# Performance work log

Hardware: AMD Instinct MI355X
Metric: run time of the kernel (lower is better)

Reference implementation:

```python
import jax, jax.numpy as jnp
import numpy as np

N_NODES = 100000


def gcn_conv(x, W, b, src, dst, deg_inv_sqrt):
    # x: [N, Cin], W: [Cin, Cout]. PyG GCNConv: transform then normalized aggregate.
    h = x @ W  # [N, Cout]
    norm = deg_inv_sqrt[src] * deg_inv_sqrt[dst]  # [E']
    msg = h[src] * norm[:, None]  # gather + scale
    out = jax.ops.segment_sum(msg, dst, num_segments=N_NODES)
    return out + b


def setup_inputs() -> dict:
    key = jax.random.key(0)
    ks = jax.random.split(key, 8)
    C = 256
    E = 3200000
    x = jax.random.normal(ks[0], (N_NODES, C), dtype=jnp.float32)
    edge_index = jax.random.randint(ks[1], (2, E), 0, N_NODES, dtype=jnp.int64)
    s = 1.0 / np.sqrt(C)
    W1 = jax.random.uniform(ks[2], (C, C), jnp.float32, -s, s)
    b1 = jnp.zeros((C,), jnp.float32)
    W2 = jax.random.uniform(ks[3], (C, C), jnp.float32, -s, s)
    b2 = jnp.zeros((C,), jnp.float32)
    Wl = jax.random.uniform(ks[4], (C, 1), jnp.float32, -s, s)
    bl = jnp.zeros((1,), jnp.float32)
    return {"x": x, "edge_index": edge_index, "W1": W1, "b1": b1,
            "W2": W2, "b2": b2, "Wl": Wl, "bl": bl}


def reference(x, edge_index, W1, b1, W2, b2, Wl, bl):
    # add self-loops once (shared by both conv layers)
    loops = jnp.arange(N_NODES, dtype=edge_index.dtype)
    src = jnp.concatenate([edge_index[0], loops])
    dst = jnp.concatenate([edge_index[1], loops])
    # symmetric normalization: deg counts incoming edges incl. self-loops
    deg = jax.ops.segment_sum(jnp.ones_like(dst, dtype=x.dtype), dst,
                              num_segments=N_NODES)
    deg_inv_sqrt = jax.lax.rsqrt(deg)  # deg >= 1 due to self-loops
    h = jax.nn.relu(gcn_conv(x, W1, b1, src, dst, deg_inv_sqrt))
    h = jax.nn.relu(gcn_conv(h, W2, b2, src, dst, deg_inv_sqrt))
    return h @ Wl + bl  # [N, 1]
```

## Files before the change

### kernel.cpp

```cpp
#include <hip/hip_runtime.h>

#define NN 100000
#define CC 256
#define EE 3200000

typedef __attribute__((ext_vector_type(8))) short bf16x8;
typedef __attribute__((ext_vector_type(4))) float f32x4;
typedef __attribute__((ext_vector_type(4))) _Float16 f16x4;

__device__ __forceinline__ float4 f4add(float4 a, float4 b) {
  return make_float4(a.x + b.x, a.y + b.y, a.z + b.z, a.w + b.w);
}

__device__ __forceinline__ unsigned short f2bf(float f) {
  unsigned u = __float_as_uint(f);
  unsigned r = (u + 0x7fffu + ((u >> 16) & 1u)) >> 16;
  return (unsigned short)r;
}
__device__ __forceinline__ float bf2f(unsigned short h) {
  return __uint_as_float(((unsigned)h) << 16);
}

__global__ void k_deg(const int* __restrict__ dst, int* __restrict__ cnt, int n) {
  int i = blockIdx.x * blockDim.x + threadIdx.x;
  int stride = gridDim.x * blockDim.x;
  for (; i < n; i += stride) {
    unsigned d = (unsigned)dst[i];
    if (d < NN) atomicAdd(&cnt[d], 1);
  }
}

__global__ void k_scan_local(const int* __restrict__ cnt, int* __restrict__ offs,
                             int* __restrict__ bsum, float* __restrict__ dis, int n) {
  __shared__ int wsum[16];
  int t = threadIdx.x;
  int idx = blockIdx.x * 1024 + t;
  int lane = t & 63, wv = t >> 6;
  int v = (idx < n) ? cnt[idx] : 0;
  if (idx < n) dis[idx] = 1.0f / sqrtf((float)(v + 1));
  int x = v;
#pragma unroll
  for (int d = 1; d < 64; d <<= 1) {
    int y = __shfl_up(x, d, 64);
    if (lane >= d) x += y;
  }
  if (lane == 63) wsum[wv] = x;
  __syncthreads();
  int wpre = 0, total = 0;
#pragma unroll
  for (int w = 0; w < 16; ++w) {
    int s = wsum[w];
    if (w < wv) wpre += s;
    total += s;
  }
  if (idx < n) offs[idx] = wpre + x - v;
  if (t == 0) bsum[blockIdx.x] = total;
}

__global__ void k_scan_bsum(const int* __restrict__ bsum, int* __restrict__ bbase, int nb) {
  __shared__ int wsum[2];
  int t = threadIdx.x;
  int lane = t & 63, wv = t >> 6;
  int v = (t < nb) ? bsum[t] : 0;
  int x = v;
#pragma unroll
  for (int d = 1; d < 64; d <<= 1) {
    int y = __shfl_up(x, d, 64);
    if (lane >= d) x += y;
  }
  if (lane == 63) wsum[wv] = x;
  __syncthreads();
  int pre = (wv == 1) ? wsum[0] : 0;
  if (t < nb) bbase[t] = pre + x - v;
  if (t == nb - 1) bbase[nb] = pre + x;
}

__global__ void k_scan_add(int* __restrict__ offs, const int* __restrict__ bbase,
                           int* __restrict__ cnt, int n, int nb) {
  int i = blockIdx.x * 256 + threadIdx.x;
  if (i < n) {
    offs[i] += bbase[i >> 10];
    cnt[i] = 0;
  }
  if (i == 0) offs[n] = bbase[nb];
}

__global__ void k_scatter(const int* __restrict__ src, const int* __restrict__ dst,
                          const int* __restrict__ offs, int* __restrict__ fill,
                          int* __restrict__ csr, int n) {
  int i = blockIdx.x * blockDim.x + threadIdx.x;
  int stride = gridDim.x * blockDim.x;
  for (; i < n; i += stride) {
    unsigned d = (unsigned)dst[i];
    unsigned s = (unsigned)src[i];
    if (d < NN && s < NN) {
      int p = offs[d] + atomicAdd(&fill[d], 1);
      csr[p] = (int)s;
    }
  }
}

__global__ void k_wsplit2(const float* __restrict__ W1, const float* __restrict__ W2,
                          unsigned short* __restrict__ W1h, unsigned short* __restrict__ W1l,
                          unsigned short* __restrict__ W2h, unsigned short* __restrict__ W2l) {
  int b = blockIdx.x, t = threadIdx.x;
  int idx = (b & 255) * 256 + t;
  int k = idx >> 8, n = idx & 255;
  if (b < 256) {
    float w = W1[k * CC + n];
    unsigned short h = f2bf(w);
    W1h[n * CC + k] = h;
    W1l[n * CC + k] = f2bf(w - bf2f(h));
  } else {
    float w = W2[k * CC + n];
    unsigned short h = f2bf(w);
    W2h[n * CC + k] = h;
    W2l[n * CC + k] = f2bf(w - bf2f(h));
  }
}

#define LDA 40

__global__ __launch_bounds__(512) void k_gemm_mfma(
    const float* __restrict__ A, const unsigned short* __restrict__ WTh,
    const unsigned short* __restrict__ WTl, const float* __restrict__ dis,
    _Float16* __restrict__ Out, int M) {
  __shared__ unsigned short Ah[128 * LDA], Al[128 * LDA];
  __shared__ unsigned short Bh[256 * LDA], Bl[256 * LDA];
  const int tid = threadIdx.x;
  const int wave = tid >> 6, lane = tid & 63;
  const int quad = lane >> 4, l16 = lane & 15;
  const int wm = wave >> 2, wn = wave & 3;
  const int row0 = blockIdx.x * 128;

  f32x4 acc[4][4];
#pragma unroll
  for (int i = 0; i < 4; ++i)
#pragma unroll
    for (int j = 0; j < 4; ++j) acc[i][j] = (f32x4){0.f, 0.f, 0.f, 0.f};

  for (int k0 = 0; k0 < CC; k0 += 32) {
#pragma unroll
    for (int q = 0; q < 2; ++q) {
      int idx = tid + 512 * q;
      int r = idx >> 3;
      int c4 = (idx & 7) << 2;
      int gr = row0 + r;
      float4 v = make_float4(0.f, 0.f, 0.f, 0.f);
      if (gr < M) v = *(const float4*)&A[(size_t)gr * CC + k0 + c4];
      ushort4 hv, lv;
      hv.x = f2bf(v.x); lv.x = f2bf(v.x - bf2f(hv.x));
      hv.y = f2bf(v.y); lv.y = f2bf(v.y - bf2f(hv.y));
      hv.z = f2bf(v.z); lv.z = f2bf(v.z - bf2f(hv.z));
      hv.w = f2bf(v.w); lv.w = f2bf(v.w - bf2f(hv.w));
      *(ushort4*)&Ah[r * LDA + c4] = hv;
      *(ushort4*)&Al[r * LDA + c4] = lv;
    }
#pragma unroll
    for (int q = 0; q < 4; ++q) {
      int idx = tid + 512 * q;
      int r = idx >> 3;
      int c4 = (idx & 7) << 2;
      const size_t g = (size_t)r * CC + k0 + c4;
      *(ushort4*)&Bh[r * LDA + c4] = *(const ushort4*)&WTh[g];
      *(ushort4*)&Bl[r * LDA + c4] = *(const ushort4*)&WTl[g];
    }
    __syncthreads();

    bf16x8 bh[4], bl[4];
#pragma unroll
    for (int j = 0; j < 4; ++j) {
      int br = (wn * 64 + j * 16 + l16) * LDA + quad * 8;
      bh[j] = *(const bf16x8*)&Bh[br];
      bl[j] = *(const bf16x8*)&Bl[br];
    }
#pragma unroll
    for (int i = 0; i < 4; ++i) {
      int ar = (wm * 64 + i * 16 + l16) * LDA + quad * 8;
      bf16x8 ah = *(const bf16x8*)&Ah[ar];
      bf16x8 al = *(const bf16x8*)&Al[ar];
#pragma unroll
      for (int j = 0; j < 4; ++j) {
        acc[i][j] = __builtin_amdgcn_mfma_f32_16x16x32_bf16(ah, bh[j], acc[i][j], 0, 0, 0);
        acc[i][j] = __builtin_amdgcn_mfma_f32_16x16x32_bf16(al, bh[j], acc[i][j], 0, 0, 0);
        acc[i][j] = __builtin_amdgcn_mfma_f32_16x16x32_bf16(ah, bl[j], acc[i][j], 0, 0, 0);
      }
    }
    __syncthreads();
  }

#pragma unroll
  for (int i = 0; i < 4; ++i) {
#pragma unroll
    for (int r4 = 0; r4 < 4; ++r4) {
      int r = row0 + wm * 64 + i * 16 + quad * 4 + r4;
      if (r < M) {
        float sc = dis[r];
#pragma unroll
        for (int j = 0; j < 4; ++j) {
          Out[(size_t)r * CC + wn * 64 + j * 16 + l16] =
              (_Float16)(acc[i][j][r4] * sc);
        }
      }
    }
  }
}

__global__ __launch_bounds__(256) void k_aggregate(
    const _Float16* __restrict__ hs, const int* __restrict__ offs,
    const int* __restrict__ csr, const float* __restrict__ dis,
    const float* __restrict__ bias, float* __restrict__ out, int n) {
  int node = blockIdx.x * 4 + (threadIdx.x >> 6);
  if (node >= n) return;
  int lane = threadIdx.x & 63;
  int c4 = lane << 2;
  int beg = offs[node], end = offs[node + 1];
  f16x4 sv = *(const f16x4*)&hs[(size_t)node * CC + c4];
  float4 a0 = make_float4((float)sv.x, (float)sv.y, (float)sv.z, (float)sv.w);
  float4 a1 = make_float4(0.f, 0.f, 0.f, 0.f);
  float4 a2 = make_float4(0.f, 0.f, 0.f, 0.f);
  float4 a3 = make_float4(0.f, 0.f, 0.f, 0.f);
  int e = beg;
  for (; e + 8 <= end; e += 8) {
    int s0 = csr[e],     s1 = csr[e + 1], s2 = csr[e + 2], s3 = csr[e + 3];
    int s4 = csr[e + 4], s5 = csr[e + 5], s6 = csr[e + 6], s7 = csr[e + 7];
    f16x4 v0 = *(const f16x4*)&hs[(size_t)s0 * CC + c4];
    f16x4 v1 = *(const f16x4*)&hs[(size_t)s1 * CC + c4];
    f16x4 v2 = *(const f16x4*)&hs[(size_t)s2 * CC + c4];
    f16x4 v3 = *(const f16x4*)&hs[(size_t)s3 * CC + c4];
    f16x4 v4 = *(const f16x4*)&hs[(size_t)s4 * CC + c4];
    f16x4 v5 = *(const f16x4*)&hs[(size_t)s5 * CC + c4];
    f16x4 v6 = *(const f16x4*)&hs[(size_t)s6 * CC + c4];
    f16x4 v7 = *(const f16x4*)&hs[(size_t)s7 * CC + c4];
    a0.x += (float)v0.x + (float)v4.x; a0.y += (float)v0.y + (float)v4.y;
    a0.z += (float)v0.z + (float)v4.z; a0.w += (float)v0.w + (float)v4.w;
    a1.x += (float)v1.x + (float)v5.x; a1.y += (float)v1.y + (float)v5.y;
    a1.z += (float)v1.z + (float)v5.z; a1.w += (float)v1.w + (float)v5.w;
    a2.x += (float)v2.x + (float)v6.x; a2.y += (float)v2.y + (float)v6.y;
    a2.z += (float)v2.z + (float)v6.z; a2.w += (float)v2.w + (float)v6.w;
    a3.x += (float)v3.x + (float)v7.x; a3.y += (float)v3.y + (float)v7.y;
    a3.z += (float)v3.z + (float)v7.z; a3.w += (float)v3.w + (float)v7.w;
  }
  for (; e + 2 <= end; e += 2) {
    int s0 = csr[e], s1 = csr[e + 1];
    f16x4 v0 = *(const f16x4*)&hs[(size_t)s0 * CC + c4];
    f16x4 v1 = *(const f16x4*)&hs[(size_t)s1 * CC + c4];
    a0.x += (float)v0.x; a0.y += (float)v0.y; a0.z += (float)v0.z; a0.w += (float)v0.w;
    a1.x += (float)v1.x; a1.y += (float)v1.y; a1.z += (float)v1.z; a1.w += (float)v1.w;
  }
  if (e < end) {
    int s0 = csr[e];
    f16x4 v0 = *(const f16x4*)&hs[(size_t)s0 * CC + c4];
    a0.x += (float)v0.x; a0.y += (float)v0.y; a0.z += (float)v0.z; a0.w += (float)v0.w;
  }
  float4 acc = f4add(f4add(a0, a1), f4add(a2, a3));
  float sc = dis[node];
  float4 bv = *(const float4*)&bias[c4];
  float4 r;
  r.x = fmaxf(acc.x * sc + bv.x, 0.f);
  r.y = fmaxf(acc.y * sc + bv.y, 0.f);
  r.z = fmaxf(acc.z * sc + bv.z, 0.f);
  r.w = fmaxf(acc.w * sc + bv.w, 0.f);
  *(float4*)&out[(size_t)node * CC + c4] = r;
}

__global__ __launch_bounds__(256) void k_aggregate_final(
    const _Float16* __restrict__ hs, const int* __restrict__ offs,
    const int* __restrict__ csr, const float* __restrict__ dis,
    const float* __restrict__ bias, const float* __restrict__ Wl,
    const float* __restrict__ bl, float* __restrict__ out, int n) {
  int node = blockIdx.x * 4 + (threadIdx.x >> 6);
  if (node >= n) return;
  int lane = threadIdx.x & 63;
  int c4 = lane << 2;
  int beg = offs[node], end = offs[node + 1];
  f16x4 sv = *(const f16x4*)&hs[(size_t)node * CC + c4];
  float4 a0 = make_float4((float)sv.x, (float)sv.y, (float)sv.z, (float)sv.w);
  float4 a1 = make_float4(0.f, 0.f, 0.f, 0.f);
  float4 a2 = make_float4(0.f, 0.f, 0.f, 0.f);
  float4 a3 = make_float4(0.f, 0.f, 0.f, 0.f);
  int e = beg;
  for (; e + 8 <= end; e += 8) {
    int s0 = csr[e],     s1 = csr[e + 1], s2 = csr[e + 2], s3 = csr[e + 3];
    int s4 = csr[e + 4], s5 = csr[e + 5], s6 = csr[e + 6], s7 = csr[e + 7];
    f16x4 v0 = *(const f16x4*)&hs[(size_t)s0 * CC + c4];
    f16x4 v1 = *(const f16x4*)&hs[(size_t)s1 * CC + c4];
    f16x4 v2 = *(const f16x4*)&hs[(size_t)s2 * CC + c4];
    f16x4 v3 = *(const f16x4*)&hs[(size_t)s3 * CC + c4];
    f16x4 v4 = *(const f16x4*)&hs[(size_t)s4 * CC + c4];
    f16x4 v5 = *(const f16x4*)&hs[(size_t)s5 * CC + c4];
    f16x4 v6 = *(const f16x4*)&hs[(size_t)s6 * CC + c4];
    f16x4 v7 = *(const f16x4*)&hs[(size_t)s7 * CC + c4];
    a0.x += (float)v0.x + (float)v4.x; a0.y += (float)v0.y + (float)v4.y;
    a0.z += (float)v0.z + (float)v4.z; a0.w += (float)v0.w + (float)v4.w;
    a1.x += (float)v1.x + (float)v5.x; a1.y += (float)v1.y + (float)v5.y;
    a1.z += (float)v1.z + (float)v5.z; a1.w += (float)v1.w + (float)v5.w;
    a2.x += (float)v2.x + (float)v6.x; a2.y += (float)v2.y + (float)v6.y;
    a2.z += (float)v2.z + (float)v6.z; a2.w += (float)v2.w + (float)v6.w;
    a3.x += (float)v3.x + (float)v7.x; a3.y += (float)v3.y + (float)v7.y;
    a3.z += (float)v3.z + (float)v7.z; a3.w += (float)v3.w + (float)v7.w;
  }
  for (; e + 2 <= end; e += 2) {
    int s0 = csr[e], s1 = csr[e + 1];
    f16x4 v0 = *(const f16x4*)&hs[(size_t)s0 * CC + c4];
    f16x4 v1 = *(const f16x4*)&hs[(size_t)s1 * CC + c4];
    a0.x += (float)v0.x; a0.y += (float)v0.y; a0.z += (float)v0.z; a0.w += (float)v0.w;
    a1.x += (float)v1.x; a1.y += (float)v1.y; a1.z += (float)v1.z; a1.w += (float)v1.w;
  }
  if (e < end) {
    int s0 = csr[e];
    f16x4 v0 = *(const f16x4*)&hs[(size_t)s0 * CC + c4];
    a0.x += (float)v0.x; a0.y += (float)v0.y; a0.z += (float)v0.z; a0.w += (float)v0.w;
  }
  float4 acc = f4add(f4add(a0, a1), f4add(a2, a3));
  float sc = dis[node];
  float4 bv = *(const float4*)&bias[c4];
  float4 w = *(const float4*)&Wl[c4];
  float s = fmaxf(acc.x * sc + bv.x, 0.f) * w.x +
            fmaxf(acc.y * sc + bv.y, 0.f) * w.y +
            fmaxf(acc.z * sc + bv.z, 0.f) * w.z +
            fmaxf(acc.w * sc + bv.w, 0.f) * w.w;
#pragma unroll
  for (int d = 32; d > 0; d >>= 1) s += __shfl_down(s, d, 64);
  if (lane == 0) out[node] = s + bl[0];
}

extern "C" void kernel_launch(void* const* d_in, const int* in_sizes, int n_in,
                              void* d_out, int out_size, void* d_ws, size_t ws_size,
                              hipStream_t stream) {
  const float* x = (const float*)d_in[0];
  const int* ei = (const int*)d_in[1];
  const float* W1 = (const float*)d_in[2];
  const float* b1 = (const float*)d_in[3];
  const float* W2 = (const float*)d_in[4];
  const float* b2 = (const float*)d_in[5];
  const float* Wl = (const float*)d_in[6];
  const float* bl = (const float*)d_in[7];
  float* out = (float*)d_out;

  const int* src = ei;
  const int* dst = ei + EE;

  char* ws = (char*)d_ws;
  size_t off = 0;
  auto alloc = [&](size_t bytes) {
    char* p = ws + off;
    off = (off + bytes + 255) & ~(size_t)255;
    return p;
  };
  float* dis = (float*)alloc((size_t)NN * 4);
  int* cnt = (int*)alloc((size_t)NN * 4);
  int* offs = (int*)alloc((size_t)(NN + 1) * 4);
  int* bsum = (int*)alloc(1024 * 4);
  int* bbase = (int*)alloc(1024 * 4);
  int* csr = (int*)alloc((size_t)EE * 4);
  unsigned short* W1h = (unsigned short*)alloc((size_t)CC * CC * 2);
  unsigned short* W1l = (unsigned short*)alloc((size_t)CC * CC * 2);
  unsigned short* W2h = (unsigned short*)alloc((size_t)CC * CC * 2);
  unsigned short* W2l = (unsigned short*)alloc((size_t)CC * CC * 2);
  _Float16* hsbuf = (_Float16*)alloc((size_t)NN * CC * 2);
  float* h1 = (float*)alloc((size_t)NN * CC * 4);

  hipMemsetAsync(cnt, 0, (size_t)NN * 4, stream);
  k_deg<<<2048, 256, 0, stream>>>(dst, cnt, EE);
  const int nb = (NN + 1023) / 1024;
  k_scan_local<<<nb, 1024, 0, stream>>>(cnt, offs, bsum, dis, NN);
  k_scan_bsum<<<1, 128, 0, stream>>>(bsum, bbase, nb);
  k_scan_add<<<(NN + 255) / 256, 256, 0, stream>>>(offs, bbase, cnt, NN, nb);
  k_scatter<<<2048, 256, 0, stream>>>(src, dst, offs, cnt, csr, EE);
  k_wsplit2<<<512, 256, 0, stream>>>(W1, W2, W1h, W1l, W2h, W2l);

  const int gblocks = (NN + 127) / 128;
  k_gemm_mfma<<<gblocks, 512, 0, stream>>>(x, W1h, W1l, dis, hsbuf, NN);
  k_aggregate<<<(NN + 3) / 4, 256, 0, stream>>>(hsbuf, offs, csr, dis, b1, h1, NN);
  k_gemm_mfma<<<gblocks, 512, 0, stream>>>(h1, W2h, W2l, dis, hsbuf, NN);
  k_aggregate_final<<<(NN + 3) / 4, 256, 0, stream>>>(hsbuf, offs, csr, dis, b2, Wl, bl, out, NN);
}
```

Measured before the change: 1.048 ms.

## Pre-split GEMM inputs to bf16 hi/lo and load MFMA operands directly from global

Adds a kernel that splits x into bf16 high/low planes and makes the first aggregation write its output directly as bf16 hi/lo pairs instead of fp32. The GEMM drops its LDS staging, barriers and in-kernel fp32-to-bf16 splitting, and loads MFMA fragments straight from global memory with row clamping. This removes per-tile conversion and sync overhead. The cost is an extra pass over x and loss of LDS reuse of the weight tile across waves, which now relies on cache hits.

```diff
diff --git a/kernel.cpp b/kernel.cpp
--- a/kernel.cpp
+++ b/kernel.cpp
@@ -119,74 +119,75 @@
   }
 }
 
-#define LDA 40
+__global__ void k_xsplit(const float* __restrict__ X, unsigned short* __restrict__ Xh,
+                         unsigned short* __restrict__ Xl, int n) {
+  int i = (blockIdx.x * 256 + threadIdx.x) * 4;
+  if (i >= n) return;
+  float4 v = *(const float4*)&X[i];
+  ushort4 h, l;
+  h.x = f2bf(v.x); l.x = f2bf(v.x - bf2f(h.x));
+  h.y = f2bf(v.y); l.y = f2bf(v.y - bf2f(h.y));
+  h.z = f2bf(v.z); l.z = f2bf(v.z - bf2f(h.z));
+  h.w = f2bf(v.w); l.w = f2bf(v.w - bf2f(h.w));
+  *(ushort4*)&Xh[i] = h;
+  *(ushort4*)&Xl[i] = l;
+}
 
 __global__ __launch_bounds__(512) void k_gemm_mfma(
-    const float* __restrict__ A, const unsigned short* __restrict__ WTh,
-    const unsigned short* __restrict__ WTl, const float* __restrict__ dis,
-    _Float16* __restrict__ Out, int M) {
-  __shared__ unsigned short Ah[128 * LDA], Al[128 * LDA];
-  __shared__ unsigned short Bh[256 * LDA], Bl[256 * LDA];
+    const unsigned short* __restrict__ Ah_g, const unsigned short* __restrict__ Al_g,
+    const unsigned short* __restrict__ WTh, const unsigned short* __restrict__ WTl,
+    const float* __restrict__ dis, _Float16* __restrict__ Out, int M) {
   const int tid = threadIdx.x;
   const int wave = tid >> 6, lane = tid & 63;
   const int quad = lane >> 4, l16 = lane & 15;
   const int wm = wave >> 2, wn = wave & 3;
   const int row0 = blockIdx.x * 128;
 
+  const unsigned short* pa_h[4];
+  const unsigned short* pa_l[4];
+#pragma unroll
+  for (int i = 0; i < 4; ++i) {
+    int r = row0 + wm * 64 + i * 16 + l16;
+    if (r > M - 1) r = M - 1;
+    pa_h[i] = &Ah_g[(size_t)r * CC + quad * 8];
+    pa_l[i] = &Al_g[(size_t)r * CC + quad * 8];
+  }
+  const unsigned short* pb_h[4];
+  const unsigned short* pb_l[4];
+#pragma unroll
+  for (int j = 0; j < 4; ++j) {
+    int nn = wn * 64 + j * 16 + l16;
+    pb_h[j] = &WTh[(size_t)nn * CC + quad * 8];
+    pb_l[j] = &WTl[(size_t)nn * CC + quad * 8];
+  }
+
   f32x4 acc[4][4];
 #pragma unroll
   for (int i = 0; i < 4; ++i)
 #pragma unroll
     for (int j = 0; j < 4; ++j) acc[i][j] = (f32x4){0.f, 0.f, 0.f, 0.f};
 
+#pragma unroll 2
   for (int k0 = 0; k0 < CC; k0 += 32) {
-#pragma unroll
-    for (int q = 0; q < 2; ++q) {
-      int idx = tid + 512 * q;
-      int r = idx >> 3;
-      int c4 = (idx & 7) << 2;
-      int gr = row0 + r;
-      float4 v = make_float4(0.f, 0.f, 0.f, 0.f);
-      if (gr < M) v = *(const float4*)&A[(size_t)gr * CC + k0 + c4];
-      ushort4 hv, lv;
-      hv.x = f2bf(v.x); lv.x = f2bf(v.x - bf2f(hv.x));
-      hv.y = f2bf(v.y); lv.y = f2bf(v.y - bf2f(hv.y));
-      hv.z = f2bf(v.z); lv.z = f2bf(v.z - bf2f(hv.z));
-      hv.w = f2bf(v.w); lv.w = f2bf(v.w - bf2f(hv.w));
-      *(ushort4*)&Ah[r * LDA + c4] = hv;
-      *(ushort4*)&Al[r * LDA + c4] = lv;
+    bf16x8 ah[4], al[4], bh[4], bl[4];
+#pragma unroll
+    for (int j = 0; j < 4; ++j) {
+      bh[j] = *(const bf16x8*)(pb_h[j] + k0);
+      bl[j] = *(const bf16x8*)(pb_l[j] + k0);
     }
 #pragma unroll
-    for (int q = 0; q < 4; ++q) {
-      int idx = tid + 512 * q;
-      int r = idx >> 3;
-      int c4 = (idx & 7) << 2;
-      const size_t g = (size_t)r * CC + k0 + c4;
-      *(ushort4*)&Bh[r * LDA + c4] = *(const ushort4*)&WTh[g];
-      *(ushort4*)&Bl[r * LDA + c4] = *(const ushort4*)&WTl[g];
+    for (int i = 0; i < 4; ++i) {
+      ah[i] = *(const bf16x8*)(pa_h[i] + k0);
+      al[i] = *(const bf16x8*)(pa_l[i] + k0);
     }
-    __syncthreads();
-
-    bf16x8 bh[4], bl[4];
-#pragma unroll
-    for (int j = 0; j < 4; ++j) {
-      int br = (wn * 64 + j * 16 + l16) * LDA + quad * 8;
-      bh[j] = *(const bf16x8*)&Bh[br];
-      bl[j] = *(const bf16x8*)&Bl[br];
-    }
-#pragma unroll
-    for (int i = 0; i < 4; ++i) {
-      int ar = (wm * 64 + i * 16 + l16) * LDA + quad * 8;
-      bf16x8 ah = *(const bf16x8*)&Ah[ar];
-      bf16x8 al = *(const bf16x8*)&Al[ar];
+#pragma unroll
+    for (int i = 0; i < 4; ++i)
 #pragma unroll
       for (int j = 0; j < 4; ++j) {
-        acc[i][j] = __builtin_amdgcn_mfma_f32_16x16x32_bf16(ah, bh[j], acc[i][j], 0, 0, 0);
-        acc[i][j] = __builtin_amdgcn_mfma_f32_16x16x32_bf16(al, bh[j], acc[i][j], 0, 0, 0);
-        acc[i][j] = __builtin_amdgcn_mfma_f32_16x16x32_bf16(ah, bl[j], acc[i][j], 0, 0, 0);
+        acc[i][j] = __builtin_amdgcn_mfma_f32_16x16x32_bf16(ah[i], bh[j], acc[i][j], 0, 0, 0);
+        acc[i][j] = __builtin_amdgcn_mfma_f32_16x16x32_bf16(al[i], bh[j], acc[i][j], 0, 0, 0);
+        acc[i][j] = __builtin_amdgcn_mfma_f32_16x16x32_bf16(ah[i], bl[j], acc[i][j], 0, 0, 0);
       }
-    }
-    __syncthreads();
   }
 
 #pragma unroll
@@ -209,7 +210,8 @@
 __global__ __launch_bounds__(256) void k_aggregate(
     const _Float16* __restrict__ hs, const int* __restrict__ offs,
     const int* __restrict__ csr, const float* __restrict__ dis,
-    const float* __restrict__ bias, float* __restrict__ out, int n) {
+    const float* __restrict__ bias, unsigned short* __restrict__ outh,
+    unsigned short* __restrict__ outl, int n) {
   int node = blockIdx.x * 4 + (threadIdx.x >> 6);
   if (node >= n) return;
   int lane = threadIdx.x & 63;
@@ -261,7 +263,13 @@
   r.y = fmaxf(acc.y * sc + bv.y, 0.f);
   r.z = fmaxf(acc.z * sc + bv.z, 0.f);
   r.w = fmaxf(acc.w * sc + bv.w, 0.f);
-  *(float4*)&out[(size_t)node * CC + c4] = r;
+  ushort4 h, l;
+  h.x = f2bf(r.x); l.x = f2bf(r.x - bf2f(h.x));
+  h.y = f2bf(r.y); l.y = f2bf(r.y - bf2f(h.y));
+  h.z = f2bf(r.z); l.z = f2bf(r.z - bf2f(h.z));
+  h.w = f2bf(r.w); l.w = f2bf(r.w - bf2f(h.w));
+  *(ushort4*)&outh[(size_t)node * CC + c4] = h;
+  *(ushort4*)&outl[(size_t)node * CC + c4] = l;
 }
 
 __global__ __launch_bounds__(256) void k_aggregate_final(
@@ -359,7 +367,8 @@
   unsigned short* W2h = (unsigned short*)alloc((size_t)CC * CC * 2);
   unsigned short* W2l = (unsigned short*)alloc((size_t)CC * CC * 2);
   _Float16* hsbuf = (_Float16*)alloc((size_t)NN * CC * 2);
-  float* h1 = (float*)alloc((size_t)NN * CC * 4);
+  unsigned short* Abh = (unsigned short*)alloc((size_t)NN * CC * 2);
+  unsigned short* Abl = (unsigned short*)alloc((size_t)NN * CC * 2);
 
   hipMemsetAsync(cnt, 0, (size_t)NN * 4, stream);
   k_deg<<<2048, 256, 0, stream>>>(dst, cnt, EE);
@@ -369,10 +378,11 @@
   k_scan_add<<<(NN + 255) / 256, 256, 0, stream>>>(offs, bbase, cnt, NN, nb);
   k_scatter<<<2048, 256, 0, stream>>>(src, dst, offs, cnt, csr, EE);
   k_wsplit2<<<512, 256, 0, stream>>>(W1, W2, W1h, W1l, W2h, W2l);
+  k_xsplit<<<(NN * CC / 4 + 255) / 256, 256, 0, stream>>>(x, Abh, Abl, NN * CC);
 
   const int gblocks = (NN + 127) / 128;
-  k_gemm_mfma<<<gblocks, 512, 0, stream>>>(x, W1h, W1l, dis, hsbuf, NN);
-  k_aggregate<<<(NN + 3) / 4, 256, 0, stream>>>(hsbuf, offs, csr, dis, b1, h1, NN);
-  k_gemm_mfma<<<gblocks, 512, 0, stream>>>(h1, W2h, W2l, dis, hsbuf, NN);
+  k_gemm_mfma<<<gblocks, 512, 0, stream>>>(Abh, Abl, W1h, W1l, dis, hsbuf, NN);
+  k_aggregate<<<(NN + 3) / 4, 256, 0, stream>>>(hsbuf, offs, csr, dis, b1, Abh, Abl, NN);
+  k_gemm_mfma<<<gblocks, 512, 0, stream>>>(Abh, Abl, W2h, W2l, dis, hsbuf, NN);
   k_aggregate_final<<<(NN + 3) / 4, 256, 0, stream>>>(hsbuf, offs, csr, dis, b2, Wl, bl, out, NN);
 }
```

After: 1.158 ms. 10.5% more time.
